# Optimization experiments

Hardware: AMD Instinct MI355X
Metric: run time of the kernel (lower is better)

The kernel has to match this reference:

```python
import jax, jax.numpy as jnp
import numpy as np

B, S, D, H, E, K = 4, 2048, 512, 2048, 8, 2


def setup_inputs() -> dict:
    key = jax.random.key(0)
    k0, k1, k2, k3 = jax.random.split(key, 4)
    return {
        "x": jax.random.normal(k0, (B, S, D), jnp.float32),
        "router_w": jax.random.normal(k1, (E, D), jnp.float32) * 0.02,
        "router_b": jnp.zeros((E,), jnp.float32),
        "w1": jax.random.normal(k2, (E, D, H), jnp.float32) * 0.02,
        "b1": jnp.zeros((E, H), jnp.float32),
        "w2": jax.random.normal(k3, (E, H, D), jnp.float32) * 0.02,
        "b2": jnp.zeros((E, D), jnp.float32),
        "top_k": K,
    }


def reference(x, router_w, router_b, w1, b1, w2, b2, top_k):
    # x: [B, S, D]; eval mode (no router noise, no dropout)
    Bb, Ss, Dd = x.shape
    Ee = w1.shape[0]
    xf = x.reshape(-1, Dd)                                   # [T, D], T = B*S
    router_logits = xf @ router_w.T + router_b               # [T, E]
    top_v, top_i = jax.lax.top_k(router_logits, top_k)       # [T, K]
    rw = jax.nn.softmax(top_v, axis=-1)                      # [T, K]
    # combine[t, e] = sum_k rw[t, k] * (top_i[t, k] == e); zero for unrouted experts
    combine = jnp.sum(jax.nn.one_hot(top_i, Ee, dtype=xf.dtype) * rw[..., None], axis=1)  # [T, E]
    out = jnp.zeros_like(xf)
    for e in range(Ee):  # fixed small expert count; each iter is a dense GEMM pair
        h = jax.nn.gelu(xf @ w1[e] + b1[e], approximate=False)  # exact erf GELU like torch nn.GELU
        y = h @ w2[e] + b2[e]                                   # [T, D]
        out = out + combine[:, e:e + 1] * y
    return out.reshape(Bb, Ss, Dd), router_logits
```

## Files before the change

kernel.cpp:

```cpp
#include <hip/hip_runtime.h>
#include <hip/hip_bf16.h>

#define TTOK 8192
#define DDIM 512
#define HDIM 2048
#define NEXP 8
#define RBLK 256
#define RTOK (TTOK / RBLK)

typedef __bf16 bf16x8 __attribute__((ext_vector_type(8)));
typedef float f32x4 __attribute__((ext_vector_type(4)));
typedef unsigned short us8 __attribute__((ext_vector_type(8)));

__device__ __forceinline__ unsigned short f2bf(float f) {
  unsigned int u = __builtin_bit_cast(unsigned int, f);
  u += 0x7fffu + ((u >> 16) & 1u);
  return (unsigned short)(u >> 16);
}

__device__ __forceinline__ void gll16(const void* g, void* l) {
  __builtin_amdgcn_global_load_lds(
      (__attribute__((address_space(1))) void*)g,
      (__attribute__((address_space(3))) void*)l, 16, 0, 0);
}

__global__ __launch_bounds__(256) void k_router(
    const float* __restrict__ x, const float* __restrict__ rw,
    const float* __restrict__ rb, float* __restrict__ logits,
    unsigned short* __restrict__ xb,
    short* __restrict__ texp, unsigned short* __restrict__ tpos,
    float* __restrict__ tgate, int* __restrict__ blockcnt) {
  __shared__ int lcnt[NEXP];
  const int tid = threadIdx.x, wid = tid >> 6, lane = tid & 63;
  if (tid < NEXP) lcnt[tid] = 0;
  __syncthreads();
  float4 w0[NEXP], w1[NEXP];
  float rbv[NEXP];
#pragma unroll
  for (int e = 0; e < NEXP; ++e) {
    const float4* wp = (const float4*)(rw + e * DDIM);
    w0[e] = wp[lane * 2];
    w1[e] = wp[lane * 2 + 1];
    rbv[e] = rb[e];
  }
  const int tbase = blockIdx.x * RTOK;
  for (int it = 0; it < RTOK / 4; ++it) {
    const int t = tbase + it * 4 + wid;
    const float4* xr = (const float4*)(x + (size_t)t * DDIM);
    float4 v0 = xr[lane * 2], v1 = xr[lane * 2 + 1];
    us8 o;
    o[0] = f2bf(v0.x); o[1] = f2bf(v0.y); o[2] = f2bf(v0.z); o[3] = f2bf(v0.w);
    o[4] = f2bf(v1.x); o[5] = f2bf(v1.y); o[6] = f2bf(v1.z); o[7] = f2bf(v1.w);
    *(us8*)(xb + (size_t)t * DDIM + lane * 8) = o;
    float a[NEXP];
#pragma unroll
    for (int e = 0; e < NEXP; ++e)
      a[e] = v0.x * w0[e].x + v0.y * w0[e].y + v0.z * w0[e].z + v0.w * w0[e].w +
             v1.x * w1[e].x + v1.y * w1[e].y + v1.z * w1[e].z + v1.w * w1[e].w;
#pragma unroll
    for (int off = 32; off > 0; off >>= 1)
#pragma unroll
      for (int e = 0; e < NEXP; ++e) a[e] += __shfl_xor(a[e], off, 64);
    if (lane == 0) {
      float lg[NEXP];
#pragma unroll
      for (int e = 0; e < NEXP; ++e) lg[e] = a[e] + rbv[e];
      float4 s0, s1;
      s0.x = lg[0]; s0.y = lg[1]; s0.z = lg[2]; s0.w = lg[3];
      s1.x = lg[4]; s1.y = lg[5]; s1.z = lg[6]; s1.w = lg[7];
      ((float4*)(logits + t * NEXP))[0] = s0;
      ((float4*)(logits + t * NEXP))[1] = s1;
      int i0 = 0; float m0 = lg[0];
#pragma unroll
      for (int e = 1; e < NEXP; ++e) if (lg[e] > m0) { m0 = lg[e]; i0 = e; }
      int i1 = 0; float m1 = -3.4e38f;
#pragma unroll
      for (int e = 0; e < NEXP; ++e) if (e != i0 && lg[e] > m1) { m1 = lg[e]; i1 = e; }
      float e1 = expf(m1 - m0);
      float inv = 1.0f / (1.0f + e1);
      int p0 = atomicAdd(&lcnt[i0], 1);
      int p1 = atomicAdd(&lcnt[i1], 1);
      texp[t * 2] = (short)i0;     tpos[t * 2] = (unsigned short)p0;     tgate[t * 2] = inv;
      texp[t * 2 + 1] = (short)i1; tpos[t * 2 + 1] = (unsigned short)p1; tgate[t * 2 + 1] = e1 * inv;
    }
  }
  __syncthreads();
  if (tid < NEXP) blockcnt[blockIdx.x * NEXP + tid] = lcnt[tid];
}

__global__ void k_offsets(const int* __restrict__ blockcnt, int* __restrict__ blockbase,
                          int* __restrict__ counts, int* __restrict__ offsets) {
  const int e = threadIdx.x;
  if (e < NEXP) {
    int run = 0;
#pragma unroll 8
    for (int b = 0; b < RBLK; ++b) {
      blockbase[b * NEXP + e] = run;
      run += blockcnt[b * NEXP + e];
    }
    counts[e] = run;
  }
  __syncthreads();
  if (e == 0) {
    int s = 0;
    for (int q = 0; q < NEXP; ++q) { offsets[q] = s; s += counts[q]; }
  }
}

__global__ void k_scatter(const short* __restrict__ texp, const unsigned short* __restrict__ tpos,
                          const float* __restrict__ tgate, const int* __restrict__ blockbase,
                          int* __restrict__ toklist, float* __restrict__ gates) {
  const int t = blockIdx.x * 256 + threadIdx.x;
  const int b = t / RTOK;
#pragma unroll
  for (int k = 0; k < 2; ++k) {
    const int e = (int)texp[t * 2 + k];
    const int pos = blockbase[b * NEXP + e] + (int)tpos[t * 2 + k];
    toklist[e * TTOK + pos] = t;
    gates[e * TTOK + pos] = tgate[t * 2 + k];
  }
}

__global__ void k_transpose2(const float* __restrict__ w1, const float* __restrict__ w2,
                             unsigned short* __restrict__ w1t, unsigned short* __restrict__ w2t) {
  __shared__ float tile[32][33];
  const int id = blockIdx.x;
  const float* in; unsigned short* out; int R, C, rem;
  if (id < 8192) {
    const int e = id >> 10; rem = id & 1023;
    R = DDIM; C = HDIM;
    in = w1 + (size_t)e * R * C; out = w1t + (size_t)e * R * C;
  } else {
    const int e = (id - 8192) >> 10; rem = (id - 8192) & 1023;
    R = HDIM; C = DDIM;
    in = w2 + (size_t)e * R * C; out = w2t + (size_t)e * R * C;
  }
  const int ctiles = C >> 5;
  const int c0 = (rem % ctiles) * 32, r0 = (rem / ctiles) * 32;
  const int tx = threadIdx.x, ty = threadIdx.y;
#pragma unroll
  for (int i = 0; i < 32; i += 8)
    tile[ty + i][tx] = in[(size_t)(r0 + ty + i) * C + (c0 + tx)];
  __syncthreads();
#pragma unroll
  for (int i = 0; i < 32; i += 8)
    out[(size_t)(c0 + ty + i) * R + (r0 + tx)] = f2bf(tile[tx][ty + i]);
}

template <int PHASE>
__global__ __launch_bounds__(256, 2) void k_gemm(
    const unsigned short* __restrict__ A, const unsigned short* __restrict__ Bt,
    const float* __restrict__ bias, const int* __restrict__ counts,
    const int* __restrict__ offsets, const int* __restrict__ toklist,
    const float* __restrict__ gates, unsigned short* __restrict__ Hout,
    float* __restrict__ Out) {
  constexpr int K = (PHASE == 1) ? DDIM : HDIM;
  constexpr int NN = (PHASE == 1) ? HDIM : DDIM;
  constexpr int KB = K * 2;
  constexpr int NX = NN / 128;
  constexpr int NXSH = (PHASE == 1) ? 4 : 2;
  constexpr int SPLITK = (PHASE == 1) ? 1 : 2;
  constexpr int KCH = K / SPLITK;
  constexpr int NT = KCH / 64;

  const int id = blockIdx.x;
  const int e = id & 7;
  int p = id >> 3;
  int s = 0;
  if (SPLITK > 1) { s = p & (SPLITK - 1); p >>= 1; }
  const int cnt = counts[e];
  const int m0 = (p >> NXSH) * 128;
  if (m0 >= cnt) return;
  const int n0 = (p & (NX - 1)) * 128;
  const int off = offsets[e];
  const int kbase = s * KCH * 2;

  __shared__ alignas(16) unsigned char smem[32768];

  const int tid = threadIdx.x;
  const int wid = tid >> 6, lane = tid & 63;

  const char* asrc[4];
  const char* bsrc[4];
  unsigned adst[4], bdst[4];
#pragma unroll
  for (int i = 0; i < 4; ++i) {
    const int c = i * 4 + wid;
    const int r = c * 8 + (lane >> 3);
    const int cs = ((lane & 7) * 16) ^ ((r & 7) << 4);
    int mrow = m0 + r; if (mrow > cnt - 1) mrow = cnt - 1;
    if (PHASE == 1) {
      const int tok = toklist[(e << 13) + mrow];
      asrc[i] = (const char*)A + (size_t)tok * (DDIM * 2) + kbase + cs;
    } else {
      asrc[i] = (const char*)A + (size_t)(off + mrow) * KB + kbase + cs;
    }
    bsrc[i] = (const char*)Bt + (size_t)e * NN * KB + (size_t)(n0 + r) * KB + kbase + cs;
    adst[i] = c * 1024;
    bdst[i] = 16384 + c * 1024;
  }

  f32x4 acc[4][4] = {};

  const int wr = wid >> 1, wc = wid & 1;
  const int lr = lane & 15, lk = lane >> 4;

  for (int t = 0; t < NT; ++t) {
    const int kb = t * 128;
#pragma unroll
    for (int i = 0; i < 4; ++i) gll16(asrc[i] + kb, smem + adst[i]);
#pragma unroll
    for (int i = 0; i < 4; ++i) gll16(bsrc[i] + kb, smem + bdst[i]);
    __syncthreads();
#pragma unroll
    for (int kk = 0; kk < 2; ++kk) {
      bf16x8 af[4], bv[4];
#pragma unroll
      for (int mi = 0; mi < 4; ++mi) {
        const int r = wr * 64 + mi * 16 + lr;
        const int byteo = r * 128 + ((kk * 64 + lk * 16) ^ ((r & 7) << 4));
        af[mi] = *(const bf16x8*)(smem + byteo);
      }
#pragma unroll
      for (int ni = 0; ni < 4; ++ni) {
        const int r = wc * 64 + ni * 16 + lr;
        const int byteo = 16384 + r * 128 + ((kk * 64 + lk * 16) ^ ((r & 7) << 4));
        bv[ni] = *(const bf16x8*)(smem + byteo);
      }
#pragma unroll
      for (int mi = 0; mi < 4; ++mi)
#pragma unroll
        for (int ni = 0; ni < 4; ++ni)
          acc[mi][ni] = __builtin_amdgcn_mfma_f32_16x16x32_bf16(af[mi], bv[ni], acc[mi][ni], 0, 0, 0);
    }
    if (t + 1 < NT) __syncthreads();
  }

  const int lq = lane >> 4;
  if (PHASE == 1) {
#pragma unroll
    for (int mi = 0; mi < 4; ++mi) {
#pragma unroll
      for (int ni = 0; ni < 4; ++ni) {
        const int n = n0 + wc * 64 + ni * 16 + lr;
        const float bv_ = bias[e * NN + n];
#pragma unroll
        for (int r2 = 0; r2 < 4; ++r2) {
          const int m = m0 + wr * 64 + mi * 16 + lq * 4 + r2;
          if (m < cnt) {
            const float xv = acc[mi][ni][r2] + bv_;
            const float g = 0.5f * xv * (1.0f + erff(xv * 0.70710678118f));
            Hout[(size_t)(off + m) * HDIM + n] = f2bf(g);
          }
        }
      }
    }
  } else {
#pragma unroll
    for (int mi = 0; mi < 4; ++mi) {
#pragma unroll
      for (int r2 = 0; r2 < 4; ++r2) {
        const int m = m0 + wr * 64 + mi * 16 + lq * 4 + r2;
        if (m < cnt) {
          const int tok = toklist[(e << 13) + m];
          const float g = gates[(e << 13) + m];
#pragma unroll
          for (int ni = 0; ni < 4; ++ni) {
            const int n = n0 + wc * 64 + ni * 16 + lr;
            const float y = acc[mi][ni][r2] + (s == 0 ? bias[e * NN + n] : 0.0f);
            atomicAdd(Out + (size_t)tok * DDIM + n, g * y);
          }
        }
      }
    }
  }
}

extern "C" void kernel_launch(void* const* d_in, const int* in_sizes, int n_in,
                              void* d_out, int out_size, void* d_ws, size_t ws_size,
                              hipStream_t stream) {
  (void)in_sizes; (void)n_in; (void)out_size; (void)ws_size;
  const float* x  = (const float*)d_in[0];
  const float* rw = (const float*)d_in[1];
  const float* rb = (const float*)d_in[2];
  const float* w1 = (const float*)d_in[3];
  const float* b1 = (const float*)d_in[4];
  const float* w2 = (const float*)d_in[5];
  const float* b2 = (const float*)d_in[6];
  float* out = (float*)d_out;
  float* logits = out + (size_t)TTOK * DDIM;

  char* ws = (char*)d_ws;
  unsigned short* xb  = (unsigned short*)(ws + 0);
  unsigned short* w1t = (unsigned short*)(ws + 8388608);
  unsigned short* w2t = (unsigned short*)(ws + 25165824);
  unsigned short* h   = (unsigned short*)(ws + 41943040);
  int*   toklist = (int*)(ws + 109051904);
  float* gates   = (float*)(ws + 109314048);
  int*   counts  = (int*)(ws + 109576192);
  int*   offsets = (int*)(ws + 109576224);
  char* rsc = ws + 41943040;
  short*          texp      = (short*)(rsc + 0);
  unsigned short* tpos      = (unsigned short*)(rsc + 32768);
  float*          tgate     = (float*)(rsc + 65536);
  int*            blockcnt  = (int*)(rsc + 131072);
  int*            blockbase = (int*)(rsc + 139264);

  hipMemsetAsync(out, 0, (size_t)TTOK * DDIM * sizeof(float), stream);

  k_router<<<RBLK, 256, 0, stream>>>(x, rw, rb, logits, xb, texp, tpos, tgate, blockcnt);
  k_transpose2<<<16384, dim3(32, 8), 0, stream>>>(w1, w2, w1t, w2t);
  k_offsets<<<1, 64, 0, stream>>>(blockcnt, blockbase, counts, offsets);
  k_scatter<<<TTOK / 256, 256, 0, stream>>>(texp, tpos, tgate, blockbase, toklist, gates);

  k_gemm<1><<<(HDIM / 128) * (TTOK / 128) * NEXP, 256, 0, stream>>>(
      xb, w1t, b1, counts, offsets, toklist, gates, h, nullptr);
  k_gemm<2><<<(DDIM / 128) * (TTOK / 128) * NEXP * 2, 256, 0, stream>>>(
      h, w2t, b2, counts, offsets, toklist, gates, nullptr, out);
}
```

Before: 333.3 us.

## Register-prefetch next K tile in expert GEMM instead of direct global-to-LDS loads

Replaces the global_load_lds direct copies with a register-staged software pipeline. The next K-slice of A and B is loaded into registers while MFMAs run on the current LDS tile, then written to LDS between two barriers. Launch bounds rise from 2 to 4 blocks per CU to raise occupancy. The change is meant to hide global memory latency behind compute, but it adds VGPR pressure under the tighter register budget and an extra barrier per iteration.

```diff
diff --git a/kernel.cpp b/kernel.cpp
--- a/kernel.cpp
+++ b/kernel.cpp
@@ -16,12 +16,6 @@
   unsigned int u = __builtin_bit_cast(unsigned int, f);
   u += 0x7fffu + ((u >> 16) & 1u);
   return (unsigned short)(u >> 16);
-}
-
-__device__ __forceinline__ void gll16(const void* g, void* l) {
-  __builtin_amdgcn_global_load_lds(
-      (__attribute__((address_space(1))) void*)g,
-      (__attribute__((address_space(3))) void*)l, 16, 0, 0);
 }
 
 __global__ __launch_bounds__(256) void k_router(
@@ -148,7 +142,7 @@
 }
 
 template <int PHASE>
-__global__ __launch_bounds__(256, 2) void k_gemm(
+__global__ __launch_bounds__(256, 4) void k_gemm(
     const unsigned short* __restrict__ A, const unsigned short* __restrict__ Bt,
     const float* __restrict__ bias, const int* __restrict__ counts,
     const int* __restrict__ offsets, const int* __restrict__ toklist,
@@ -199,19 +193,32 @@
     adst[i] = c * 1024;
     bdst[i] = 16384 + c * 1024;
   }
+  const unsigned lofs = (unsigned)lane * 16;
 
   f32x4 acc[4][4] = {};
 
   const int wr = wid >> 1, wc = wid & 1;
   const int lr = lane & 15, lk = lane >> 4;
 
+  uint4 ar[4], br[4];
+#pragma unroll
+  for (int i = 0; i < 4; ++i) { ar[i] = *(const uint4*)(asrc[i]); br[i] = *(const uint4*)(bsrc[i]); }
+#pragma unroll
+  for (int i = 0; i < 4; ++i) {
+    *(uint4*)(smem + adst[i] + lofs) = ar[i];
+    *(uint4*)(smem + bdst[i] + lofs) = br[i];
+  }
+  __syncthreads();
+
   for (int t = 0; t < NT; ++t) {
-    const int kb = t * 128;
-#pragma unroll
-    for (int i = 0; i < 4; ++i) gll16(asrc[i] + kb, smem + adst[i]);
-#pragma unroll
-    for (int i = 0; i < 4; ++i) gll16(bsrc[i] + kb, smem + bdst[i]);
-    __syncthreads();
+    if (t + 1 < NT) {
+      const int kb = (t + 1) * 128;
+#pragma unroll
+      for (int i = 0; i < 4; ++i) {
+        ar[i] = *(const uint4*)(asrc[i] + kb);
+        br[i] = *(const uint4*)(bsrc[i] + kb);
+      }
+    }
 #pragma unroll
     for (int kk = 0; kk < 2; ++kk) {
       bf16x8 af[4], bv[4];
@@ -233,7 +240,15 @@
         for (int ni = 0; ni < 4; ++ni)
           acc[mi][ni] = __builtin_amdgcn_mfma_f32_16x16x32_bf16(af[mi], bv[ni], acc[mi][ni], 0, 0, 0);
     }
-    if (t + 1 < NT) __syncthreads();
+    if (t + 1 < NT) {
+      __syncthreads();
+#pragma unroll
+      for (int i = 0; i < 4; ++i) {
+        *(uint4*)(smem + adst[i] + lofs) = ar[i];
+        *(uint4*)(smem + bdst[i] + lofs) = br[i];
+      }
+      __syncthreads();
+    }
   }
 
   const int lq = lane >> 4;
```

Result: slower. 555.8 us (+66.8%).

## Replace split-K atomic scatter in down-projection with bf16 staging and combine kernel

Applied to the files above, without the earlier changes.

The second expert GEMM no longer uses split-K and no longer atomically adds gated outputs into the output tensor. It uses 64-row M tiles, writes per-slot bf16 results into a staging buffer (reusing the w1t workspace), and a new combine kernel gathers each token's two expert rows and applies the gates with plain stores. This removes the output memset and the float atomic traffic, at the cost of an extra kernel launch, an extra round trip of intermediate data through memory, and bf16 rounding of the per-expert outputs.

```diff
diff --git a/kernel.cpp b/kernel.cpp
--- a/kernel.cpp
+++ b/kernel.cpp
@@ -109,7 +109,9 @@
 
 __global__ void k_scatter(const short* __restrict__ texp, const unsigned short* __restrict__ tpos,
                           const float* __restrict__ tgate, const int* __restrict__ blockbase,
-                          int* __restrict__ toklist, float* __restrict__ gates) {
+                          const int* __restrict__ offsets,
+                          int* __restrict__ toklist, int* __restrict__ cidx,
+                          float* __restrict__ cgate) {
   const int t = blockIdx.x * 256 + threadIdx.x;
   const int b = t / RTOK;
 #pragma unroll
@@ -117,7 +119,8 @@
     const int e = (int)texp[t * 2 + k];
     const int pos = blockbase[b * NEXP + e] + (int)tpos[t * 2 + k];
     toklist[e * TTOK + pos] = t;
-    gates[e * TTOK + pos] = tgate[t * 2 + k];
+    cidx[t * 2 + k] = offsets[e] + pos;
+    cgate[t * 2 + k] = tgate[t * 2 + k];
   }
 }
 
@@ -152,55 +155,60 @@
     const unsigned short* __restrict__ A, const unsigned short* __restrict__ Bt,
     const float* __restrict__ bias, const int* __restrict__ counts,
     const int* __restrict__ offsets, const int* __restrict__ toklist,
-    const float* __restrict__ gates, unsigned short* __restrict__ Hout,
-    float* __restrict__ Out) {
+    unsigned short* __restrict__ Out) {
   constexpr int K = (PHASE == 1) ? DDIM : HDIM;
   constexpr int NN = (PHASE == 1) ? HDIM : DDIM;
   constexpr int KB = K * 2;
   constexpr int NX = NN / 128;
   constexpr int NXSH = (PHASE == 1) ? 4 : 2;
-  constexpr int SPLITK = (PHASE == 1) ? 1 : 2;
-  constexpr int KCH = K / SPLITK;
-  constexpr int NT = KCH / 64;
+  constexpr int BM = (PHASE == 1) ? 128 : 64;
+  constexpr int AI = BM / 32;
+  constexpr int MI = BM / 32;
+  constexpr int WRM = BM / 2;
+  constexpr int ASZ = BM * 128;
+  constexpr int NT = K / 64;
 
   const int id = blockIdx.x;
   const int e = id & 7;
-  int p = id >> 3;
-  int s = 0;
-  if (SPLITK > 1) { s = p & (SPLITK - 1); p >>= 1; }
+  const int p = id >> 3;
   const int cnt = counts[e];
-  const int m0 = (p >> NXSH) * 128;
+  const int m0 = (p >> NXSH) * BM;
   if (m0 >= cnt) return;
   const int n0 = (p & (NX - 1)) * 128;
   const int off = offsets[e];
-  const int kbase = s * KCH * 2;
-
-  __shared__ alignas(16) unsigned char smem[32768];
+
+  __shared__ alignas(16) unsigned char smem[ASZ + 16384];
 
   const int tid = threadIdx.x;
   const int wid = tid >> 6, lane = tid & 63;
 
-  const char* asrc[4];
+  const char* asrc[AI];
   const char* bsrc[4];
-  unsigned adst[4], bdst[4];
-#pragma unroll
-  for (int i = 0; i < 4; ++i) {
+  unsigned adst[AI], bdst[4];
+#pragma unroll
+  for (int i = 0; i < AI; ++i) {
     const int c = i * 4 + wid;
     const int r = c * 8 + (lane >> 3);
     const int cs = ((lane & 7) * 16) ^ ((r & 7) << 4);
     int mrow = m0 + r; if (mrow > cnt - 1) mrow = cnt - 1;
     if (PHASE == 1) {
       const int tok = toklist[(e << 13) + mrow];
-      asrc[i] = (const char*)A + (size_t)tok * (DDIM * 2) + kbase + cs;
+      asrc[i] = (const char*)A + (size_t)tok * (DDIM * 2) + cs;
     } else {
-      asrc[i] = (const char*)A + (size_t)(off + mrow) * KB + kbase + cs;
-    }
-    bsrc[i] = (const char*)Bt + (size_t)e * NN * KB + (size_t)(n0 + r) * KB + kbase + cs;
+      asrc[i] = (const char*)A + (size_t)(off + mrow) * KB + cs;
+    }
     adst[i] = c * 1024;
-    bdst[i] = 16384 + c * 1024;
-  }
-
-  f32x4 acc[4][4] = {};
+  }
+#pragma unroll
+  for (int i = 0; i < 4; ++i) {
+    const int c = i * 4 + wid;
+    const int r = c * 8 + (lane >> 3);
+    const int cs = ((lane & 7) * 16) ^ ((r & 7) << 4);
+    bsrc[i] = (const char*)Bt + (size_t)e * NN * KB + (size_t)(n0 + r) * KB + cs;
+    bdst[i] = ASZ + c * 1024;
+  }
+
+  f32x4 acc[MI][4] = {};
 
   const int wr = wid >> 1, wc = wid & 1;
   const int lr = lane & 15, lk = lane >> 4;
@@ -208,27 +216,27 @@
   for (int t = 0; t < NT; ++t) {
     const int kb = t * 128;
 #pragma unroll
-    for (int i = 0; i < 4; ++i) gll16(asrc[i] + kb, smem + adst[i]);
+    for (int i = 0; i < AI; ++i) gll16(asrc[i] + kb, smem + adst[i]);
 #pragma unroll
     for (int i = 0; i < 4; ++i) gll16(bsrc[i] + kb, smem + bdst[i]);
     __syncthreads();
 #pragma unroll
     for (int kk = 0; kk < 2; ++kk) {
-      bf16x8 af[4], bv[4];
-#pragma unroll
-      for (int mi = 0; mi < 4; ++mi) {
-        const int r = wr * 64 + mi * 16 + lr;
+      bf16x8 af[MI], bv[4];
+#pragma unroll
+      for (int mi = 0; mi < MI; ++mi) {
+        const int r = wr * WRM + mi * 16 + lr;
         const int byteo = r * 128 + ((kk * 64 + lk * 16) ^ ((r & 7) << 4));
         af[mi] = *(const bf16x8*)(smem + byteo);
       }
 #pragma unroll
       for (int ni = 0; ni < 4; ++ni) {
         const int r = wc * 64 + ni * 16 + lr;
-        const int byteo = 16384 + r * 128 + ((kk * 64 + lk * 16) ^ ((r & 7) << 4));
+        const int byteo = ASZ + r * 128 + ((kk * 64 + lk * 16) ^ ((r & 7) << 4));
         bv[ni] = *(const bf16x8*)(smem + byteo);
       }
 #pragma unroll
-      for (int mi = 0; mi < 4; ++mi)
+      for (int mi = 0; mi < MI; ++mi)
 #pragma unroll
         for (int ni = 0; ni < 4; ++ni)
           acc[mi][ni] = __builtin_amdgcn_mfma_f32_16x16x32_bf16(af[mi], bv[ni], acc[mi][ni], 0, 0, 0);
@@ -237,43 +245,49 @@
   }
 
   const int lq = lane >> 4;
-  if (PHASE == 1) {
-#pragma unroll
-    for (int mi = 0; mi < 4; ++mi) {
-#pragma unroll
-      for (int ni = 0; ni < 4; ++ni) {
-        const int n = n0 + wc * 64 + ni * 16 + lr;
-        const float bv_ = bias[e * NN + n];
-#pragma unroll
-        for (int r2 = 0; r2 < 4; ++r2) {
-          const int m = m0 + wr * 64 + mi * 16 + lq * 4 + r2;
-          if (m < cnt) {
+#pragma unroll
+  for (int mi = 0; mi < MI; ++mi) {
+#pragma unroll
+    for (int ni = 0; ni < 4; ++ni) {
+      const int n = n0 + wc * 64 + ni * 16 + lr;
+      const float bv_ = bias[e * NN + n];
+#pragma unroll
+      for (int r2 = 0; r2 < 4; ++r2) {
+        const int m = m0 + wr * WRM + mi * 16 + lq * 4 + r2;
+        if (m < cnt) {
+          if (PHASE == 1) {
             const float xv = acc[mi][ni][r2] + bv_;
             const float g = 0.5f * xv * (1.0f + erff(xv * 0.70710678118f));
-            Hout[(size_t)(off + m) * HDIM + n] = f2bf(g);
+            Out[(size_t)(off + m) * HDIM + n] = f2bf(g);
+          } else {
+            Out[(size_t)(off + m) * DDIM + n] = f2bf(acc[mi][ni][r2] + bv_);
           }
         }
       }
     }
-  } else {
-#pragma unroll
-    for (int mi = 0; mi < 4; ++mi) {
-#pragma unroll
-      for (int r2 = 0; r2 < 4; ++r2) {
-        const int m = m0 + wr * 64 + mi * 16 + lq * 4 + r2;
-        if (m < cnt) {
-          const int tok = toklist[(e << 13) + m];
-          const float g = gates[(e << 13) + m];
-#pragma unroll
-          for (int ni = 0; ni < 4; ++ni) {
-            const int n = n0 + wc * 64 + ni * 16 + lr;
-            const float y = acc[mi][ni][r2] + (s == 0 ? bias[e * NN + n] : 0.0f);
-            atomicAdd(Out + (size_t)tok * DDIM + n, g * y);
-          }
-        }
-      }
-    }
-  }
+  }
+}
+
+__global__ __launch_bounds__(256) void k_combine(const unsigned short* __restrict__ yp,
+                                                 const int* __restrict__ cidx,
+                                                 const float* __restrict__ cgate,
+                                                 float* __restrict__ out) {
+  const int t = blockIdx.x * 4 + (threadIdx.x >> 6);
+  const int lane = threadIdx.x & 63;
+  const int i0 = cidx[t * 2], i1 = cidx[t * 2 + 1];
+  const float g0 = cgate[t * 2], g1 = cgate[t * 2 + 1];
+  us8 a = *(const us8*)(yp + (size_t)i0 * DDIM + lane * 8);
+  us8 b = *(const us8*)(yp + (size_t)i1 * DDIM + lane * 8);
+  float o[8];
+#pragma unroll
+  for (int j = 0; j < 8; ++j) {
+    const float va = __builtin_bit_cast(float, (unsigned)a[j] << 16);
+    const float vb = __builtin_bit_cast(float, (unsigned)b[j] << 16);
+    o[j] = g0 * va + g1 * vb;
+  }
+  float* op = out + (size_t)t * DDIM + lane * 8;
+  *(float4*)op = *(float4*)o;
+  *(float4*)(op + 4) = *(float4*)(o + 4);
 }
 
 extern "C" void kernel_launch(void* const* d_in, const int* in_sizes, int n_in,
@@ -296,9 +310,11 @@
   unsigned short* w2t = (unsigned short*)(ws + 25165824);
   unsigned short* h   = (unsigned short*)(ws + 41943040);
   int*   toklist = (int*)(ws + 109051904);
-  float* gates   = (float*)(ws + 109314048);
-  int*   counts  = (int*)(ws + 109576192);
-  int*   offsets = (int*)(ws + 109576224);
+  int*   cidx    = (int*)(ws + 109314048);
+  float* cgate   = (float*)(ws + 109379584);
+  int*   counts  = (int*)(ws + 109445120);
+  int*   offsets = (int*)(ws + 109445152);
+  unsigned short* yp = w1t;
   char* rsc = ws + 41943040;
   short*          texp      = (short*)(rsc + 0);
   unsigned short* tpos      = (unsigned short*)(rsc + 32768);
@@ -306,15 +322,15 @@
   int*            blockcnt  = (int*)(rsc + 131072);
   int*            blockbase = (int*)(rsc + 139264);
 
-  hipMemsetAsync(out, 0, (size_t)TTOK * DDIM * sizeof(float), stream);
-
   k_router<<<RBLK, 256, 0, stream>>>(x, rw, rb, logits, xb, texp, tpos, tgate, blockcnt);
   k_transpose2<<<16384, dim3(32, 8), 0, stream>>>(w1, w2, w1t, w2t);
   k_offsets<<<1, 64, 0, stream>>>(blockcnt, blockbase, counts, offsets);
-  k_scatter<<<TTOK / 256, 256, 0, stream>>>(texp, tpos, tgate, blockbase, toklist, gates);
+  k_scatter<<<TTOK / 256, 256, 0, stream>>>(texp, tpos, tgate, blockbase, offsets,
+                                            toklist, cidx, cgate);
 
   k_gemm<1><<<(HDIM / 128) * (TTOK / 128) * NEXP, 256, 0, stream>>>(
-      xb, w1t, b1, counts, offsets, toklist, gates, h, nullptr);
-  k_gemm<2><<<(DDIM / 128) * (TTOK / 128) * NEXP * 2, 256, 0, stream>>>(
-      h, w2t, b2, counts, offsets, toklist, gates, nullptr, out);
-}
+      xb, w1t, b1, counts, offsets, toklist, h);
+  k_gemm<2><<<(DDIM / 128) * (TTOK / 64) * NEXP, 256, 0, stream>>>(
+      h, w2t, b2, counts, offsets, nullptr, yp);
+  k_combine<<<TTOK / 4, 256, 0, stream>>>(yp, cidx, cgate, out);
+}
```

After: 277.3 us. -16.8%, faster.
